# Kernel optimization log

Hardware: AMD Instinct MI355X
Metric: run time of the kernel (lower is better)

Reference implementation:

```python
import jax, jax.numpy as jnp
import numpy as np

B, S, HID = 32, 577, 768
NH, HD = 12, 64  # num heads, head dim (HID = NH*HD)


def setup_inputs() -> dict:
    key = jax.random.key(0)
    ks = jax.random.split(key, 8)
    scale = 1.0 / np.sqrt(HID)
    return {
        "hidden_states": jax.random.normal(ks[0], (B, S, HID), jnp.float32),
        "lateral_states": jax.random.normal(ks[1], (B, NH, S, HD), jnp.float32),
        "Wq": jax.random.normal(ks[2], (HID, HID), jnp.float32) * scale,
        "bq": jax.random.normal(ks[3], (HID,), jnp.float32) * 0.02,
        "Wk": jax.random.normal(ks[4], (HID, HID), jnp.float32) * scale,
        "bk": jax.random.normal(ks[5], (HID,), jnp.float32) * 0.02,
        "Wv": jax.random.normal(ks[6], (HID, HID), jnp.float32) * scale,
        "bv": jax.random.normal(ks[7], (HID,), jnp.float32) * 0.02,
        "mix_with": 0,  # 0 -> 'q', 1 -> 'k', 2 -> 'v'
    }


def _heads(x):
    # [B, S, HID] -> [B, NH, S, HD]
    return x.reshape(B, S, NH, HD).transpose(0, 2, 1, 3)


def reference(hidden_states, lateral_states, Wq, bq, Wk, bk, Wv, bv, mix_with):
    q = _heads(hidden_states @ Wq.T + bq)
    k = _heads(hidden_states @ Wk.T + bk)
    v = _heads(hidden_states @ Wv.T + bv)
    if mix_with == 0:
        q = q * lateral_states
    elif mix_with == 1:
        k = k * lateral_states
    elif mix_with == 2:
        v = v * lateral_states
    else:
        raise ValueError("mix_with must be 0 (q), 1 (k), or 2 (v)")
    scores = jnp.einsum("bhqd,bhkd->bhqk", q, k) / jnp.sqrt(jnp.float32(HD))
    probs = jax.nn.softmax(scores, axis=-1)
    ctx = jnp.einsum("bhqk,bhkd->bhqd", probs, v)
    # [B, NH, S, HD] -> [B, S, HID]
    return ctx.transpose(0, 2, 1, 3).reshape(B, S, HID)
```

## Files before the change

### kernel.cpp

```cpp
#include <hip/hip_runtime.h>

#define B_    32
#define S_    577
#define HID_  768
#define NH_   12
#define HD_   64
#define SPAD  640
#define SB_   5
#define MT_   160
#define KT_   12
#define NT_   18

typedef __attribute__((ext_vector_type(8))) short short8;
typedef __attribute__((ext_vector_type(4))) short short4s;
typedef __attribute__((ext_vector_type(4))) float float4_;

static __device__ __forceinline__ float bf2f(short s) {
    union { float f; unsigned u; } cvt;
    cvt.u = ((unsigned)(unsigned short)s) << 16;
    return cvt.f;
}
static __device__ __forceinline__ short f2bf(float f) {
    union { float f; unsigned u; } cvt;
    cvt.f = f;
    unsigned u = cvt.u;
    unsigned r = u + 0x7FFF + ((u >> 16) & 1);
    return (short)(r >> 16);
}
static __device__ __forceinline__ void gl_lds16(const short* g, short* l) {
    __builtin_amdgcn_global_load_lds(
        (const __attribute__((address_space(1))) unsigned int*)g,
        (__attribute__((address_space(3))) unsigned int*)l,
        16, 0, 0);
}

__global__ __launch_bounds__(256) void convA_kernel(
    const float* __restrict__ X, short* __restrict__ ximg)
{
    const int mt = blockIdx.x, kt = blockIdx.y;
    const int b = mt / SB_, sb = mt - b * SB_;
    short* img = ximg + ((size_t)mt * KT_ + kt) * 8192;
#pragma unroll
    for (int i = 0; i < 4; ++i) {
        const int j = i * 256 + threadIdx.x;
        const int row = j >> 3, kg = j & 7;
        const int s = sb * 128 + row;
        const int srow = (s < S_) ? s : 0;
        const float* src = X + ((size_t)b * S_ + srow) * HID_ + kt * 64 + kg * 8;
        float4_ f0 = *(const float4_*)src;
        float4_ f1 = *(const float4_*)(src + 4);
        short8 s8;
#pragma unroll
        for (int e = 0; e < 4; ++e) { s8[e] = f2bf(f0[e]); s8[e + 4] = f2bf(f1[e]); }
        *(short8*)(img + ((size_t)kg * 128 + row) * 8) = s8;
    }
}

__global__ __launch_bounds__(256) void convB_kernel(
    const float* __restrict__ Wq, const float* __restrict__ Wk,
    const float* __restrict__ Wv, short* __restrict__ wimg)
{
    const int nt = blockIdx.x, kt = blockIdx.y;
    const int z = nt / 6;
    const float* W = (z == 0) ? Wq : (z == 1) ? Wk : Wv;
    const int n0 = (nt - z * 6) * 128;
    short* img = wimg + ((size_t)nt * KT_ + kt) * 8192;
#pragma unroll
    for (int i = 0; i < 4; ++i) {
        const int j = i * 256 + threadIdx.x;
        const int row = j >> 3, kg = j & 7;
        const float* src = W + (size_t)(n0 + row) * HID_ + kt * 64 + kg * 8;
        float4_ f0 = *(const float4_*)src;
        float4_ f1 = *(const float4_*)(src + 4);
        short8 s8;
#pragma unroll
        for (int e = 0; e < 4; ++e) { s8[e] = f2bf(f0[e]); s8[e + 4] = f2bf(f1[e]); }
        *(short8*)(img + ((size_t)kg * 128 + row) * 8) = s8;
    }
}

__global__ __launch_bounds__(256) void gemm_kernel(
    const short* __restrict__ ximg, const short* __restrict__ wimg,
    const float* __restrict__ bq, const float* __restrict__ bk,
    const float* __restrict__ bv,
    const float* __restrict__ lat, const int* __restrict__ mixw,
    short* __restrict__ qo, short* __restrict__ ko, short* __restrict__ vo)
{
    __shared__ __align__(16) short lds[32768];

    const int nt = blockIdx.x;
    const int mt = blockIdx.y;
    const int z   = nt / 6;
    const int nz0 = (nt - z * 6) * 128;
    const int b   = mt / SB_;
    const int s0  = (mt - b * SB_) * 128;

    const int tid  = threadIdx.x;
    const int wave = tid >> 6;
    const int lane = tid & 63;
    const int quad = lane >> 4;
    const int l16  = lane & 15;

    const short* ag = ximg + ((size_t)mt * KT_) * 8192;
    const short* bg = wimg + ((size_t)nt * KT_) * 8192;

    float4_ acc[4][4] = {};
    const int r0 = (wave & 1) * 64 + l16;
    const int c0 = (wave >> 1) * 64 + l16;

#pragma unroll
    for (int i = 0; i < 4; ++i) {
        gl_lds16(ag + (i * 256 + tid) * 8, lds + (i * 256 + wave * 64) * 8);
        gl_lds16(bg + (i * 256 + tid) * 8, lds + 16384 + (i * 256 + wave * 64) * 8);
    }

    for (int kt = 0; kt < KT_; ++kt) {
        __syncthreads();
        const int cur = kt & 1;
        if (kt + 1 < KT_) {
            short* Ad = lds + (cur ^ 1) * 8192;
            short* Bd = lds + 16384 + (cur ^ 1) * 8192;
            const short* an = ag + (size_t)(kt + 1) * 8192;
            const short* bn = bg + (size_t)(kt + 1) * 8192;
#pragma unroll
            for (int i = 0; i < 4; ++i) {
                gl_lds16(an + (i * 256 + tid) * 8, Ad + (i * 256 + wave * 64) * 8);
                gl_lds16(bn + (i * 256 + tid) * 8, Bd + (i * 256 + wave * 64) * 8);
            }
        }
        const short* Ab = lds + cur * 8192;
        const short* Bb = lds + 16384 + cur * 8192;
#pragma unroll
        for (int c = 0; c < 2; ++c) {
            const int kb = (c * 4 + quad) * 128;
            short8 af[4], bf[4];
#pragma unroll
            for (int mi = 0; mi < 4; ++mi)
                af[mi] = *(const short8*)(Ab + (kb + r0 + mi * 16) * 8);
#pragma unroll
            for (int g = 0; g < 4; ++g)
                bf[g] = *(const short8*)(Bb + (kb + c0 + g * 16) * 8);
#pragma unroll
            for (int mi = 0; mi < 4; ++mi)
#pragma unroll
                for (int g = 0; g < 4; ++g)
                    acc[mi][g] = __builtin_amdgcn_mfma_f32_16x16x32_bf16(
                        af[mi], bf[g], acc[mi][g], 0, 0, 0);
        }
    }
    __syncthreads();

    const int mwv = *mixw;
    const float* bb = (z == 0) ? bq : (z == 1) ? bk : bv;
    const int hh   = (nz0 + (wave >> 1) * 64) >> 6;
    const size_t bh = (size_t)b * NH_ + hh;
    const int sW   = s0 + (wave & 1) * 64;
    const int ch   = sW >> 6;
    short* P = lds + wave * 4608;

    if (z < 2) {
#pragma unroll
        for (int mi = 0; mi < 4; ++mi)
#pragma unroll
            for (int i = 0; i < 4; ++i) {
                const int ml = mi * 16 + quad * 4 + i;
                const int s  = sW + ml;
                const float* lp =
                    lat + (bh * S_ + (s < S_ ? s : S_ - 1)) * HD_;
#pragma unroll
                for (int g = 0; g < 4; ++g) {
                    const int d = g * 16 + l16;
                    float val = acc[mi][g][i] + bb[hh * 64 + d];
                    if (z == mwv) val *= lp[d];
                    P[ml * 72 + d] = f2bf(val);
                }
            }
    } else {
#pragma unroll
        for (int mi = 0; mi < 4; ++mi)
#pragma unroll
            for (int g = 0; g < 4; ++g) {
                const int d  = g * 16 + l16;
                const int mb = mi * 16 + quad * 4;
                short4s w;
#pragma unroll
                for (int i = 0; i < 4; ++i) {
                    const int s = sW + mb + i;
                    float val = acc[mi][g][i] + bb[hh * 64 + d];
                    if (mwv == 2)
                        val *= lat[(bh * S_ + (s < S_ ? s : S_ - 1)) * HD_ + d];
                    w[i] = f2bf(val);
                }
                *(short4s*)(P + d * 72 + mb) = w;
            }
    }
    __syncthreads();

    const int rr = lane >> 3, cc = lane & 7;
    if (z == 0) {
        short* qb = qo + (size_t)bh * SPAD * HD_;
#pragma unroll
        for (int j = 0; j < 8; ++j) {
            const int r = j * 8 + rr;
            *(short8*)(qb + (size_t)(sW + r) * 64 + cc * 8) =
                *(const short8*)(P + r * 72 + cc * 8);
        }
    } else if (z == 1) {
        short* kb = ko + ((size_t)bh * 10 + ch) * 4096;
#pragma unroll
        for (int j = 0; j < 8; ++j) {
            const int r = j * 8 + rr;
            *(short8*)(kb + (cc * 64 + r) * 8) =
                *(const short8*)(P + r * 72 + cc * 8);
        }
    } else {
        short* vb = vo + ((size_t)bh * 10 + ch) * 4096;
#pragma unroll
        for (int j = 0; j < 8; ++j) {
            const int r = j * 8 + rr;
            *(short8*)(vb + (cc * 64 + r) * 8) =
                *(const short8*)(P + r * 72 + cc * 8);
        }
    }
}

__global__ __launch_bounds__(256) void attn_kernel(
    const short* __restrict__ q, const short* __restrict__ k,
    const short* __restrict__ vt, float* __restrict__ out)
{
    __shared__ __align__(16) short Kt[4096];
    __shared__ __align__(16) short Vt[4096];
    __shared__ __align__(16) short pbuf[4][16][64];

    const int bh   = blockIdx.x;
    const int b    = bh / NH_;
    const int h    = bh - b * NH_;
    const int tid  = threadIdx.x;
    const int wave = tid >> 6;
    const int lane = tid & 63;
    const int quad = lane >> 4;
    const int l16  = lane & 15;
    const int q0   = blockIdx.y * 64 + wave * 16;

    const short* qp   = q  + (size_t)bh * SPAD * HD_;
    const short* kimg = k  + (size_t)bh * 40960;
    const short* vimg = vt + (size_t)bh * 40960;

    const short8 aq0 = *(const short8*)(qp + (size_t)(q0 + l16) * HD_ + quad * 8);
    const short8 aq1 = *(const short8*)(qp + (size_t)(q0 + l16) * HD_ + 32 + quad * 8);

    float m_i[4], l_i[4];
    float4_ O[4] = {};
#pragma unroll
    for (int i = 0; i < 4; ++i) { m_i[i] = -3.0e38f; l_i[i] = 0.0f; }

    for (int kc = 0; kc < 10; ++kc) {
        const int key0 = kc * 64;
        if (kc) __syncthreads();
#pragma unroll
        for (int i = 0; i < 2; ++i) {
            gl_lds16(kimg + (size_t)kc * 4096 + (i * 256 + tid) * 8,
                     Kt + (i * 256 + wave * 64) * 8);
            gl_lds16(vimg + (size_t)kc * 4096 + (i * 256 + tid) * 8,
                     Vt + (i * 256 + wave * 64) * 8);
        }
        __syncthreads();

        float4_ sc[4] = {};
#pragma unroll
        for (int c = 0; c < 2; ++c) {
            const int kb = (c * 4 + quad) * 64;
            const short8 aq = c ? aq1 : aq0;
#pragma unroll
            for (int g = 0; g < 4; ++g) {
                short8 bk8 = *(const short8*)(Kt + (kb + g * 16 + l16) * 8);
                sc[g] = __builtin_amdgcn_mfma_f32_16x16x32_bf16(aq, bk8, sc[g], 0, 0, 0);
            }
        }

        float kmask[4];
#pragma unroll
        for (int g = 0; g < 4; ++g)
            kmask[g] = (key0 + g * 16 + l16 < S_) ? 0.0f : -3.0e38f;

        float alpha[4];
#pragma unroll
        for (int i = 0; i < 4; ++i) {
            float s0 = sc[0][i] * 0.125f + kmask[0];
            float s1 = sc[1][i] * 0.125f + kmask[1];
            float s2 = sc[2][i] * 0.125f + kmask[2];
            float s3 = sc[3][i] * 0.125f + kmask[3];
            float cm = fmaxf(fmaxf(s0, s1), fmaxf(s2, s3));
#pragma unroll
            for (int off = 1; off < 16; off <<= 1)
                cm = fmaxf(cm, __shfl_xor(cm, off));
            const float mn = fmaxf(m_i[i], cm);
            alpha[i] = __expf(m_i[i] - mn);
            m_i[i] = mn;
            const short p0 = f2bf(__expf(s0 - mn));
            const short p1 = f2bf(__expf(s1 - mn));
            const short p2 = f2bf(__expf(s2 - mn));
            const short p3 = f2bf(__expf(s3 - mn));
            pbuf[wave][quad * 4 + i][l16]      = p0;
            pbuf[wave][quad * 4 + i][l16 + 16] = p1;
            pbuf[wave][quad * 4 + i][l16 + 32] = p2;
            pbuf[wave][quad * 4 + i][l16 + 48] = p3;
            float rs = (bf2f(p0) + bf2f(p1)) + (bf2f(p2) + bf2f(p3));
#pragma unroll
            for (int off = 1; off < 16; off <<= 1)
                rs += __shfl_xor(rs, off);
            l_i[i] = l_i[i] * alpha[i] + rs;
        }

#pragma unroll
        for (int g = 0; g < 4; ++g)
#pragma unroll
            for (int i = 0; i < 4; ++i) O[g][i] *= alpha[i];

#pragma unroll
        for (int c = 0; c < 2; ++c) {
            const short8 ap = *(const short8*)(&pbuf[wave][l16][c * 32 + quad * 8]);
            const int kb = (c * 4 + quad) * 64;
#pragma unroll
            for (int g = 0; g < 4; ++g) {
                short8 bv8 = *(const short8*)(Vt + (kb + g * 16 + l16) * 8);
                O[g] = __builtin_amdgcn_mfma_f32_16x16x32_bf16(ap, bv8, O[g], 0, 0, 0);
            }
        }
    }

#pragma unroll
    for (int i = 0; i < 4; ++i) {
        const int s = q0 + quad * 4 + i;
        if (s >= S_) continue;
        const float inv = 1.0f / l_i[i];
#pragma unroll
        for (int g = 0; g < 4; ++g)
            out[((size_t)b * S_ + s) * HID_ + h * HD_ + g * 16 + l16] = O[g][i] * inv;
    }
}

extern "C" void kernel_launch(void* const* d_in, const int* in_sizes, int n_in,
                              void* d_out, int out_size, void* d_ws, size_t ws_size,
                              hipStream_t stream) {
    (void)in_sizes; (void)n_in; (void)out_size; (void)ws_size;

    const float* X   = (const float*)d_in[0];
    const float* lat = (const float*)d_in[1];
    const float* Wq  = (const float*)d_in[2];
    const float* bq  = (const float*)d_in[3];
    const float* Wk  = (const float*)d_in[4];
    const float* bk  = (const float*)d_in[5];
    const float* Wv  = (const float*)d_in[6];
    const float* bv  = (const float*)d_in[7];
    const int* mixw  = (const int*)d_in[8];
    float* out = (float*)d_out;

    const size_t per = (size_t)B_ * NH_ * SPAD * HD_;
    short* qw   = (short*)d_ws;
    short* kw   = qw + per;
    short* vw   = kw + per;
    short* wimg = vw + per;
    short* ximg = wimg + (size_t)NT_ * KT_ * 8192;

    convA_kernel<<<dim3(MT_, KT_), 256, 0, stream>>>(X, ximg);
    convB_kernel<<<dim3(NT_, KT_), 256, 0, stream>>>(Wq, Wk, Wv, wimg);
    gemm_kernel<<<dim3(NT_, MT_), 256, 0, stream>>>(
        ximg, wimg, bq, bk, bv, lat, mixw, qw, kw, vw);
    attn_kernel<<<dim3(384, 10), 256, 0, stream>>>(qw, kw, vw, out);
}
```

Measured before the change: 443.0 us.

## Deepen GEMM and attention load pipelines with explicit vmcnt waits and XCD-aware block swizzle

The GEMM K loop now works in half-tile stages and keeps three stages of global-to-LDS loads in flight. It syncs with explicit s_waitcnt vmcnt counts and raw s_barrier in place of __syncthreads, and raises wave priority around the MFMA bursts. The GEMM grid becomes 1D with a block-id remap so that consecutive blocks on the same XCD share A/B tiles. Attention double-buffers its K/V LDS tiles so the next chunk loads while the current one is computed, at the cost of twice the LDS and hand-counted waits that must match the number of issued loads.

```diff
diff --git a/kernel.cpp b/kernel.cpp
--- a/kernel.cpp
+++ b/kernel.cpp
@@ -15,6 +15,8 @@
 typedef __attribute__((ext_vector_type(4))) short short4s;
 typedef __attribute__((ext_vector_type(4))) float float4_;
 
+#define WAITV(n) asm volatile("s_waitcnt vmcnt(" #n ")" ::: "memory")
+
 static __device__ __forceinline__ float bf2f(short s) {
     union { float f; unsigned u; } cvt;
     cvt.u = ((unsigned)(unsigned short)s) << 16;
@@ -88,8 +90,11 @@
 {
     __shared__ __align__(16) short lds[32768];
 
-    const int nt = blockIdx.x;
-    const int mt = blockIdx.y;
+    const int bid0 = blockIdx.x;
+    const int bids = (bid0 & 7) * 360 + (bid0 >> 3);
+    const int mt = bids / NT_;
+    const int nt = bids - mt * NT_;
+
     const int z   = nt / 6;
     const int nz0 = (nt - z * 6) * 128;
     const int b   = mt / SB_;
@@ -108,47 +113,53 @@
     const int r0 = (wave & 1) * 64 + l16;
     const int c0 = (wave >> 1) * 64 + l16;
 
-#pragma unroll
-    for (int i = 0; i < 4; ++i) {
-        gl_lds16(ag + (i * 256 + tid) * 8, lds + (i * 256 + wave * 64) * 8);
-        gl_lds16(bg + (i * 256 + tid) * 8, lds + 16384 + (i * 256 + wave * 64) * 8);
-    }
-
-    for (int kt = 0; kt < KT_; ++kt) {
-        __syncthreads();
-        const int cur = kt & 1;
-        if (kt + 1 < KT_) {
-            short* Ad = lds + (cur ^ 1) * 8192;
-            short* Bd = lds + 16384 + (cur ^ 1) * 8192;
-            const short* an = ag + (size_t)(kt + 1) * 8192;
-            const short* bn = bg + (size_t)(kt + 1) * 8192;
-#pragma unroll
-            for (int i = 0; i < 4; ++i) {
-                gl_lds16(an + (i * 256 + tid) * 8, Ad + (i * 256 + wave * 64) * 8);
-                gl_lds16(bn + (i * 256 + tid) * 8, Bd + (i * 256 + wave * 64) * 8);
-            }
-        }
-        const short* Ab = lds + cur * 8192;
-        const short* Bb = lds + 16384 + cur * 8192;
-#pragma unroll
-        for (int c = 0; c < 2; ++c) {
-            const int kb = (c * 4 + quad) * 128;
-            short8 af[4], bf[4];
-#pragma unroll
-            for (int mi = 0; mi < 4; ++mi)
-                af[mi] = *(const short8*)(Ab + (kb + r0 + mi * 16) * 8);
+    auto STAGE = [&](int P) {
+        const int kt = P >> 1, h = P & 1;
+        const size_t off = (size_t)kt * 8192 + h * 4096;
+        const short* as = ag + off;
+        const short* bs = bg + off;
+        short* Ad = lds + ((kt & 1) * 8192 + h * 4096);
+        short* Bd = lds + 16384 + ((kt & 1) * 8192 + h * 4096);
+#pragma unroll
+        for (int i = 0; i < 2; ++i) {
+            gl_lds16(as + (i * 256 + tid) * 8, Ad + (i * 256 + wave * 64) * 8);
+            gl_lds16(bs + (i * 256 + tid) * 8, Bd + (i * 256 + wave * 64) * 8);
+        }
+    };
+
+    STAGE(0); STAGE(1); STAGE(2);
+
+    for (int P = 0; P < 2 * KT_; ++P) {
+        if (P < 2 * KT_ - 3) STAGE(P + 3);
+        if (P < 2 * KT_ - 3)      { WAITV(12); }
+        else if (P == 2 * KT_ - 3){ WAITV(8);  }
+        else if (P == 2 * KT_ - 2){ WAITV(4);  }
+        else                      { WAITV(0);  }
+        __builtin_amdgcn_sched_barrier(0);
+        __builtin_amdgcn_s_barrier();
+        __builtin_amdgcn_sched_barrier(0);
+
+        const short* Ab = lds + ((P >> 1) & 1) * 8192;
+        const short* Bb = lds + 16384 + ((P >> 1) & 1) * 8192;
+        const int kb = ((P & 1) * 4 + quad) * 128;
+        short8 af[4], bf4[4];
+#pragma unroll
+        for (int mi = 0; mi < 4; ++mi)
+            af[mi] = *(const short8*)(Ab + (kb + r0 + mi * 16) * 8);
+#pragma unroll
+        for (int g = 0; g < 4; ++g)
+            bf4[g] = *(const short8*)(Bb + (kb + c0 + g * 16) * 8);
+        __builtin_amdgcn_s_setprio(1);
+#pragma unroll
+        for (int mi = 0; mi < 4; ++mi)
 #pragma unroll
             for (int g = 0; g < 4; ++g)
-                bf[g] = *(const short8*)(Bb + (kb + c0 + g * 16) * 8);
-#pragma unroll
-            for (int mi = 0; mi < 4; ++mi)
-#pragma unroll
-                for (int g = 0; g < 4; ++g)
-                    acc[mi][g] = __builtin_amdgcn_mfma_f32_16x16x32_bf16(
-                        af[mi], bf[g], acc[mi][g], 0, 0, 0);
-        }
-    }
-    __syncthreads();
+                acc[mi][g] = __builtin_amdgcn_mfma_f32_16x16x32_bf16(
+                    af[mi], bf4[g], acc[mi][g], 0, 0, 0);
+        __builtin_amdgcn_s_setprio(0);
+        __builtin_amdgcn_sched_barrier(0);
+        __builtin_amdgcn_s_barrier();
+    }
 
     const int mwv = *mixw;
     const float* bb = (z == 0) ? bq : (z == 1) ? bk : bv;
@@ -228,8 +239,8 @@
     const short* __restrict__ q, const short* __restrict__ k,
     const short* __restrict__ vt, float* __restrict__ out)
 {
-    __shared__ __align__(16) short Kt[4096];
-    __shared__ __align__(16) short Vt[4096];
+    __shared__ __align__(16) short Kt[2][4096];
+    __shared__ __align__(16) short Vt[2][4096];
     __shared__ __align__(16) short pbuf[4][16][64];
 
     const int bh   = blockIdx.x;
@@ -249,34 +260,47 @@
     const short8 aq0 = *(const short8*)(qp + (size_t)(q0 + l16) * HD_ + quad * 8);
     const short8 aq1 = *(const short8*)(qp + (size_t)(q0 + l16) * HD_ + 32 + quad * 8);
 
+    auto STAGE = [&](int kc) {
+#pragma unroll
+        for (int i = 0; i < 2; ++i) {
+            gl_lds16(kimg + (size_t)kc * 4096 + (i * 256 + tid) * 8,
+                     Kt[kc & 1] + (i * 256 + wave * 64) * 8);
+            gl_lds16(vimg + (size_t)kc * 4096 + (i * 256 + tid) * 8,
+                     Vt[kc & 1] + (i * 256 + wave * 64) * 8);
+        }
+    };
+
     float m_i[4], l_i[4];
     float4_ O[4] = {};
 #pragma unroll
     for (int i = 0; i < 4; ++i) { m_i[i] = -3.0e38f; l_i[i] = 0.0f; }
 
+    STAGE(0);
+
     for (int kc = 0; kc < 10; ++kc) {
         const int key0 = kc * 64;
-        if (kc) __syncthreads();
-#pragma unroll
-        for (int i = 0; i < 2; ++i) {
-            gl_lds16(kimg + (size_t)kc * 4096 + (i * 256 + tid) * 8,
-                     Kt + (i * 256 + wave * 64) * 8);
-            gl_lds16(vimg + (size_t)kc * 4096 + (i * 256 + tid) * 8,
-                     Vt + (i * 256 + wave * 64) * 8);
-        }
-        __syncthreads();
+        if (kc < 9) STAGE(kc + 1);
+        if (kc < 9) { WAITV(4); } else { WAITV(0); }
+        __builtin_amdgcn_sched_barrier(0);
+        __builtin_amdgcn_s_barrier();
+        __builtin_amdgcn_sched_barrier(0);
+
+        const short* Kb = Kt[kc & 1];
+        const short* Vb = Vt[kc & 1];
 
         float4_ sc[4] = {};
+        __builtin_amdgcn_s_setprio(1);
 #pragma unroll
         for (int c = 0; c < 2; ++c) {
             const int kb = (c * 4 + quad) * 64;
             const short8 aq = c ? aq1 : aq0;
 #pragma unroll
             for (int g = 0; g < 4; ++g) {
-                short8 bk8 = *(const short8*)(Kt + (kb + g * 16 + l16) * 8);
+                short8 bk8 = *(const short8*)(Kb + (kb + g * 16 + l16) * 8);
                 sc[g] = __builtin_amdgcn_mfma_f32_16x16x32_bf16(aq, bk8, sc[g], 0, 0, 0);
             }
         }
+        __builtin_amdgcn_s_setprio(0);
 
         float kmask[4];
 #pragma unroll
@@ -317,16 +341,20 @@
 #pragma unroll
             for (int i = 0; i < 4; ++i) O[g][i] *= alpha[i];
 
+        __builtin_amdgcn_s_setprio(1);
 #pragma unroll
         for (int c = 0; c < 2; ++c) {
             const short8 ap = *(const short8*)(&pbuf[wave][l16][c * 32 + quad * 8]);
             const int kb = (c * 4 + quad) * 64;
 #pragma unroll
             for (int g = 0; g < 4; ++g) {
-                short8 bv8 = *(const short8*)(Vt + (kb + g * 16 + l16) * 8);
+                short8 bv8 = *(const short8*)(Vb + (kb + g * 16 + l16) * 8);
                 O[g] = __builtin_amdgcn_mfma_f32_16x16x32_bf16(ap, bv8, O[g], 0, 0, 0);
             }
         }
+        __builtin_amdgcn_s_setprio(0);
+        __builtin_amdgcn_sched_barrier(0);
+        __builtin_amdgcn_s_barrier();
     }
 
 #pragma unroll
@@ -365,7 +393,7 @@
 
     convA_kernel<<<dim3(MT_, KT_), 256, 0, stream>>>(X, ximg);
     convB_kernel<<<dim3(NT_, KT_), 256, 0, stream>>>(Wq, Wk, Wv, wimg);
-    gemm_kernel<<<dim3(NT_, MT_), 256, 0, stream>>>(
+    gemm_kernel<<<dim3(NT_ * MT_), 256, 0, stream>>>(
         ximg, wimg, bq, bk, bv, lat, mixw, qw, kw, vw);
     attn_kernel<<<dim3(384, 10), 256, 0, stream>>>(qw, kw, vw, out);
 }
```

Measured after the change: 447.9 us. About the same (+1.1%).

## Read GEMM and attention operands directly from global, remap blocks across XCDs

Applied to the files above, without the earlier changes.

Both the projection GEMM and the attention kernel stop staging A/B and K/V tiles through LDS and instead load MFMA fragments straight from global memory, dropping the LDS buffers and barriers. Linear block IDs are remapped so consecutive work lands on the same XCD (stride-8 swizzle) to improve L2 reuse. MFMA sections are wrapped with s_setprio. The cost is more global/L2 traffic and latency exposure per wave with no double buffering, relying on caches to serve repeated reads.

```diff
diff --git a/kernel.cpp b/kernel.cpp
--- a/kernel.cpp
+++ b/kernel.cpp
@@ -27,12 +27,6 @@
     unsigned r = u + 0x7FFF + ((u >> 16) & 1);
     return (short)(r >> 16);
 }
-static __device__ __forceinline__ void gl_lds16(const short* g, short* l) {
-    __builtin_amdgcn_global_load_lds(
-        (const __attribute__((address_space(1))) unsigned int*)g,
-        (__attribute__((address_space(3))) unsigned int*)l,
-        16, 0, 0);
-}
 
 __global__ __launch_bounds__(256) void convA_kernel(
     const float* __restrict__ X, short* __restrict__ ximg)
@@ -86,10 +80,13 @@
     const float* __restrict__ lat, const int* __restrict__ mixw,
     short* __restrict__ qo, short* __restrict__ ko, short* __restrict__ vo)
 {
-    __shared__ __align__(16) short lds[32768];
-
-    const int nt = blockIdx.x;
-    const int mt = blockIdx.y;
+    __shared__ __align__(16) short eP[4][4608];
+
+    const int bid0 = blockIdx.x;
+    const int bids = (bid0 & 7) * 360 + (bid0 >> 3);
+    const int mt = bids / NT_;
+    const int nt = bids - mt * NT_;
+
     const int z   = nt / 6;
     const int nz0 = (nt - z * 6) * 128;
     const int b   = mt / SB_;
@@ -108,47 +105,29 @@
     const int r0 = (wave & 1) * 64 + l16;
     const int c0 = (wave >> 1) * 64 + l16;
 
-#pragma unroll
-    for (int i = 0; i < 4; ++i) {
-        gl_lds16(ag + (i * 256 + tid) * 8, lds + (i * 256 + wave * 64) * 8);
-        gl_lds16(bg + (i * 256 + tid) * 8, lds + 16384 + (i * 256 + wave * 64) * 8);
-    }
-
     for (int kt = 0; kt < KT_; ++kt) {
-        __syncthreads();
-        const int cur = kt & 1;
-        if (kt + 1 < KT_) {
-            short* Ad = lds + (cur ^ 1) * 8192;
-            short* Bd = lds + 16384 + (cur ^ 1) * 8192;
-            const short* an = ag + (size_t)(kt + 1) * 8192;
-            const short* bn = bg + (size_t)(kt + 1) * 8192;
-#pragma unroll
-            for (int i = 0; i < 4; ++i) {
-                gl_lds16(an + (i * 256 + tid) * 8, Ad + (i * 256 + wave * 64) * 8);
-                gl_lds16(bn + (i * 256 + tid) * 8, Bd + (i * 256 + wave * 64) * 8);
-            }
-        }
-        const short* Ab = lds + cur * 8192;
-        const short* Bb = lds + 16384 + cur * 8192;
+        const short* ak = ag + (size_t)kt * 8192;
+        const short* bk8p = bg + (size_t)kt * 8192;
 #pragma unroll
         for (int c = 0; c < 2; ++c) {
             const int kb = (c * 4 + quad) * 128;
-            short8 af[4], bf[4];
+            short8 af[4], bf4[4];
 #pragma unroll
             for (int mi = 0; mi < 4; ++mi)
-                af[mi] = *(const short8*)(Ab + (kb + r0 + mi * 16) * 8);
-#pragma unroll
-            for (int g = 0; g < 4; ++g)
-                bf[g] = *(const short8*)(Bb + (kb + c0 + g * 16) * 8);
+                af[mi] = *(const short8*)(ak + (kb + r0 + mi * 16) * 8);
+#pragma unroll
+            for (int g = 0; g < 4; ++g)
+                bf4[g] = *(const short8*)(bk8p + (kb + c0 + g * 16) * 8);
+            __builtin_amdgcn_s_setprio(1);
 #pragma unroll
             for (int mi = 0; mi < 4; ++mi)
 #pragma unroll
                 for (int g = 0; g < 4; ++g)
                     acc[mi][g] = __builtin_amdgcn_mfma_f32_16x16x32_bf16(
-                        af[mi], bf[g], acc[mi][g], 0, 0, 0);
-        }
-    }
-    __syncthreads();
+                        af[mi], bf4[g], acc[mi][g], 0, 0, 0);
+            __builtin_amdgcn_s_setprio(0);
+        }
+    }
 
     const int mwv = *mixw;
     const float* bb = (z == 0) ? bq : (z == 1) ? bk : bv;
@@ -156,7 +135,7 @@
     const size_t bh = (size_t)b * NH_ + hh;
     const int sW   = s0 + (wave & 1) * 64;
     const int ch   = sW >> 6;
-    short* P = lds + wave * 4608;
+    short* P = eP[wave];
 
     if (z < 2) {
 #pragma unroll
@@ -194,7 +173,6 @@
                 *(short4s*)(P + d * 72 + mb) = w;
             }
     }
-    __syncthreads();
 
     const int rr = lane >> 3, cc = lane & 7;
     if (z == 0) {
@@ -228,11 +206,13 @@
     const short* __restrict__ q, const short* __restrict__ k,
     const short* __restrict__ vt, float* __restrict__ out)
 {
-    __shared__ __align__(16) short Kt[4096];
-    __shared__ __align__(16) short Vt[4096];
     __shared__ __align__(16) short pbuf[4][16][64];
 
-    const int bh   = blockIdx.x;
+    const int bid0 = blockIdx.x;
+    const int bids = (bid0 & 7) * 480 + (bid0 >> 3);
+    const int bh = bids / 10;
+    const int qt = bids - bh * 10;
+
     const int b    = bh / NH_;
     const int h    = bh - b * NH_;
     const int tid  = threadIdx.x;
@@ -240,7 +220,7 @@
     const int lane = tid & 63;
     const int quad = lane >> 4;
     const int l16  = lane & 15;
-    const int q0   = blockIdx.y * 64 + wave * 16;
+    const int q0   = qt * 64 + wave * 16;
 
     const short* qp   = q  + (size_t)bh * SPAD * HD_;
     const short* kimg = k  + (size_t)bh * 40960;
@@ -256,26 +236,23 @@
 
     for (int kc = 0; kc < 10; ++kc) {
         const int key0 = kc * 64;
-        if (kc) __syncthreads();
-#pragma unroll
-        for (int i = 0; i < 2; ++i) {
-            gl_lds16(kimg + (size_t)kc * 4096 + (i * 256 + tid) * 8,
-                     Kt + (i * 256 + wave * 64) * 8);
-            gl_lds16(vimg + (size_t)kc * 4096 + (i * 256 + tid) * 8,
-                     Vt + (i * 256 + wave * 64) * 8);
-        }
-        __syncthreads();
+        const short* Kc = kimg + (size_t)kc * 4096;
+        const short* Vc = vimg + (size_t)kc * 4096;
 
         float4_ sc[4] = {};
 #pragma unroll
         for (int c = 0; c < 2; ++c) {
             const int kb = (c * 4 + quad) * 64;
             const short8 aq = c ? aq1 : aq0;
-#pragma unroll
-            for (int g = 0; g < 4; ++g) {
-                short8 bk8 = *(const short8*)(Kt + (kb + g * 16 + l16) * 8);
-                sc[g] = __builtin_amdgcn_mfma_f32_16x16x32_bf16(aq, bk8, sc[g], 0, 0, 0);
-            }
+            short8 bk8[4];
+#pragma unroll
+            for (int g = 0; g < 4; ++g)
+                bk8[g] = *(const short8*)(Kc + (kb + g * 16 + l16) * 8);
+            __builtin_amdgcn_s_setprio(1);
+#pragma unroll
+            for (int g = 0; g < 4; ++g)
+                sc[g] = __builtin_amdgcn_mfma_f32_16x16x32_bf16(aq, bk8[g], sc[g], 0, 0, 0);
+            __builtin_amdgcn_s_setprio(0);
         }
 
         float kmask[4];
@@ -321,11 +298,15 @@
         for (int c = 0; c < 2; ++c) {
             const short8 ap = *(const short8*)(&pbuf[wave][l16][c * 32 + quad * 8]);
             const int kb = (c * 4 + quad) * 64;
-#pragma unroll
-            for (int g = 0; g < 4; ++g) {
-                short8 bv8 = *(const short8*)(Vt + (kb + g * 16 + l16) * 8);
-                O[g] = __builtin_amdgcn_mfma_f32_16x16x32_bf16(ap, bv8, O[g], 0, 0, 0);
-            }
+            short8 bv8[4];
+#pragma unroll
+            for (int g = 0; g < 4; ++g)
+                bv8[g] = *(const short8*)(Vc + (kb + g * 16 + l16) * 8);
+            __builtin_amdgcn_s_setprio(1);
+#pragma unroll
+            for (int g = 0; g < 4; ++g)
+                O[g] = __builtin_amdgcn_mfma_f32_16x16x32_bf16(ap, bv8[g], O[g], 0, 0, 0);
+            __builtin_amdgcn_s_setprio(0);
         }
     }
 
@@ -365,7 +346,7 @@
 
     convA_kernel<<<dim3(MT_, KT_), 256, 0, stream>>>(X, ximg);
     convB_kernel<<<dim3(NT_, KT_), 256, 0, stream>>>(Wq, Wk, Wv, wimg);
-    gemm_kernel<<<dim3(NT_, MT_), 256, 0, stream>>>(
+    gemm_kernel<<<dim3(NT_ * MT_), 256, 0, stream>>>(
         ximg, wimg, bq, bk, bv, lat, mixw, qw, kw, vw);
-    attn_kernel<<<dim3(384, 10), 256, 0, stream>>>(qw, kw, vw, out);
-}
+    attn_kernel<<<dim3(3840), 256, 0, stream>>>(qw, kw, vw, out);
+}
```

Result: faster. 406.5 us (-8.2%).
